# Kernel optimization log

Hardware: AMD Instinct MI355X
Metric: run time of the kernel (lower is better)

## Reference

```python
import jax, jax.numpy as jnp
import numpy as np

D_IN = 1024
D_OUT = 1024
NUM_HEADS = 16
HEAD_DIM = D_OUT // NUM_HEADS


def setup_inputs() -> dict:
    key = jax.random.key(0)
    ks = jax.random.split(key, 9)
    s = 0.02
    return {
        "x": jax.random.normal(ks[0], (2, 2048, D_IN), dtype=jnp.float32),
        "Wq": jax.random.normal(ks[1], (D_IN, D_OUT), dtype=jnp.float32) * s,
        "bq": jnp.zeros((D_OUT,), dtype=jnp.float32),
        "Wk": jax.random.normal(ks[2], (D_IN, D_OUT), dtype=jnp.float32) * s,
        "bk": jnp.zeros((D_OUT,), dtype=jnp.float32),
        "Wv": jax.random.normal(ks[3], (D_IN, D_OUT), dtype=jnp.float32) * s,
        "bv": jnp.zeros((D_OUT,), dtype=jnp.float32),
        "Wo": jax.random.normal(ks[4], (D_OUT, D_OUT), dtype=jnp.float32) * s,
        "bo": jnp.zeros((D_OUT,), dtype=jnp.float32),
    }


def reference(x, Wq, bq, Wk, bk, Wv, bv, Wo, bo):
    B, S, _ = x.shape
    H, Dh = NUM_HEADS, HEAD_DIM
    q = (x @ Wq + bq).reshape(B, S, H, Dh).transpose(0, 2, 1, 3)  # bhsd
    k = (x @ Wk + bk).reshape(B, S, H, Dh).transpose(0, 2, 1, 3)
    v = (x @ Wv + bv).reshape(B, S, H, Dh).transpose(0, 2, 1, 3)
    scores = jnp.einsum("bhqd,bhkd->bhqk", q, k) * (Dh ** -0.5)
    causal = jnp.tril(jnp.ones((S, S), dtype=bool))
    scores = jnp.where(causal, scores, jnp.float32(-jnp.inf))
    w = jax.nn.softmax(scores, axis=-1)
    ctx = jnp.einsum("bhqk,bhkd->bhqd", w, v)
    ctx = ctx.transpose(0, 2, 1, 3).reshape(B, S, H * Dh)
    return ctx @ Wo + bo
```

## Files before the change

kernel.cpp:

```cpp
#include <hip/hip_runtime.h>
#include <cmath>

#define D_IN 1024
#define D_OUT 1024
#define NUM_HEADS 16
#define HEAD_DIM 64
#define BATCH 2
#define SEQ 2048
#define GK 1024
#define KT 32
#define NT_K (GK / 64)

typedef __attribute__((ext_vector_type(8))) short short8;
typedef __attribute__((ext_vector_type(4))) short short4v;
typedef __attribute__((ext_vector_type(4))) float float4v;
typedef __attribute__((ext_vector_type(16))) float f32x16;
typedef __attribute__((ext_vector_type(2))) int int2v;

__device__ __forceinline__ unsigned short f2bf(float f) {
  unsigned int u = __builtin_bit_cast(unsigned int, f);
  unsigned int r = (u + 0x7FFFu + ((u >> 16) & 1u)) >> 16;
  return (unsigned short)r;
}
__device__ __forceinline__ float bf2f(unsigned short h) {
  return __builtin_bit_cast(float, (unsigned int)h << 16);
}

__device__ __forceinline__ unsigned int cvtpk(float lo, float hi) {
  unsigned int r;
  asm("v_cvt_pk_bf16_f32 %0, %1, %2" : "=v"(r) : "v"(lo), "v"(hi));
  return r;
}

__device__ __forceinline__ void async_copy16(void* lds, const void* g) {
  __builtin_amdgcn_global_load_lds(
      (const __attribute__((address_space(1))) unsigned int*)g,
      (__attribute__((address_space(3))) unsigned int*)lds, 16, 0, 0);
}

__global__ __launch_bounds__(256) void prep(
    const float* __restrict__ x, const float* __restrict__ Wq,
    const float* __restrict__ Wk, const float* __restrict__ Wv,
    const float* __restrict__ Wo, unsigned short* __restrict__ xb,
    unsigned short* __restrict__ wqkv_t, unsigned short* __restrict__ wo_t) {
  const int z = blockIdx.z;
  if (z == 4) {
    const int bid = blockIdx.y * 32 + blockIdx.x;
    const size_t i0 = ((size_t)bid * 256 + threadIdx.x) * 16;
#pragma unroll
    for (int half = 0; half < 2; ++half) {
      const size_t o = i0 + half * 8;
      float4 a = *(const float4*)(x + o);
      float4 b = *(const float4*)(x + o + 4);
      union { unsigned int d[4]; short8 v; } t;
      t.d[0] = cvtpk(a.x, a.y); t.d[1] = cvtpk(a.z, a.w);
      t.d[2] = cvtpk(b.x, b.y); t.d[3] = cvtpk(b.z, b.w);
      *(short8*)(xb + o) = t.v;
    }
    return;
  }
  const float* W = (z == 0) ? Wq : (z == 1) ? Wk : (z == 2) ? Wv : Wo;
  unsigned short* out = (z < 3) ? (wqkv_t + (size_t)z * 1024 * 1024) : wo_t;

  __shared__ float T[32][33];
  const int r = threadIdx.x >> 3;
  const int c4 = (threadIdx.x & 7) << 2;
  const int k0 = blockIdx.x * 32, n0 = blockIdx.y * 32;

  float4 v = *(const float4*)(W + (size_t)(k0 + r) * 1024 + n0 + c4);
  T[r][c4 + 0] = v.x; T[r][c4 + 1] = v.y; T[r][c4 + 2] = v.z; T[r][c4 + 3] = v.w;
  __syncthreads();

  union { unsigned short u[4]; short4v v4; } o;
#pragma unroll
  for (int i = 0; i < 4; ++i) o.u[i] = f2bf(T[c4 + i][r]);
  *(short4v*)(out + (size_t)(n0 + r) * 1024 + k0 + c4) = o.v4;
}

__device__ __forceinline__ void stage_tile(
    const unsigned short* __restrict__ A, const unsigned short* __restrict__ Bt,
    unsigned short* S, int buf, int bm, int bn, int k0, int wave, int lane) {
  unsigned short* As = S + buf * 16384;
  unsigned short* Bs = As + 8192;
#pragma unroll
  for (int t = 0; t < 4; ++t) {
    const int c = (wave * 4 + t) * 64 + lane;
    const int srow = c >> 3;
    const int sgc = ((c & 7) ^ (srow & 7)) * 8;
    async_copy16(As + (size_t)c * 8, A + (size_t)(bm + srow) * GK + k0 + sgc);
  }
#pragma unroll
  for (int t = 0; t < 4; ++t) {
    const int c = (wave * 4 + t) * 64 + lane;
    const int srow = c >> 3;
    const int sgc = ((c & 7) ^ (srow & 7)) * 8;
    async_copy16(Bs + (size_t)c * 8, Bt + (size_t)(bn + srow) * GK + k0 + sgc);
  }
}

__device__ __forceinline__ void gemm_core(
    const unsigned short* __restrict__ A, const unsigned short* __restrict__ Bt,
    unsigned short* S, int bm, int bn, float4v acc[4][4]) {
  const int tid = threadIdx.x;
  const int wave = tid >> 6, lane = tid & 63;
  const int quad = lane >> 4, l16 = lane & 15;
  const int wr = wave >> 1, wc = wave & 1;
  const int sw = l16 & 7;

  stage_tile(A, Bt, S, 0, bm, bn, 0, wave, lane);

  for (int t = 0; t < NT_K; ++t) {
    if (t + 1 < NT_K) {
      stage_tile(A, Bt, S, (t + 1) & 1, bm, bn, (t + 1) * 64, wave, lane);
      asm volatile("s_waitcnt vmcnt(8)" ::: "memory");
    } else {
      asm volatile("s_waitcnt vmcnt(0)" ::: "memory");
    }
    __builtin_amdgcn_sched_barrier(0);
    __builtin_amdgcn_s_barrier();
    __builtin_amdgcn_sched_barrier(0);

    const unsigned short* Asc = S + (t & 1) * 16384;
    const unsigned short* Bsc = Asc + 8192;
#pragma unroll
    for (int h = 0; h < 2; ++h) {
      short8 af[4], bfr[4];
#pragma unroll
      for (int i = 0; i < 4; ++i) {
        const int row = wr * 64 + i * 16 + l16;
        af[i] = *(const short8*)&Asc[((size_t)row * 8 + ((h * 4 + quad) ^ sw)) * 8];
      }
#pragma unroll
      for (int j = 0; j < 4; ++j) {
        const int row = wc * 64 + j * 16 + l16;
        bfr[j] = *(const short8*)&Bsc[((size_t)row * 8 + ((h * 4 + quad) ^ sw)) * 8];
      }
#pragma unroll
      for (int i = 0; i < 4; ++i)
#pragma unroll
        for (int j = 0; j < 4; ++j)
          acc[i][j] = __builtin_amdgcn_mfma_f32_16x16x32_bf16(af[i], bfr[j], acc[i][j], 0, 0, 0);
    }

    __builtin_amdgcn_sched_barrier(0);
    __builtin_amdgcn_s_barrier();
    __builtin_amdgcn_sched_barrier(0);
  }
}

__global__ __launch_bounds__(256) void gemm_qkv(
    const unsigned short* __restrict__ A, const unsigned short* __restrict__ Bt,
    const float* __restrict__ bq, const float* __restrict__ bk,
    const float* __restrict__ bv,
    unsigned short* __restrict__ qbuf, unsigned short* __restrict__ kblk,
    unsigned short* __restrict__ vblk) {
  __shared__ unsigned short SMEM[2 * 128 * 64 * 2];
  const int tid = threadIdx.x;
  const int wave = tid >> 6, lane = tid & 63;
  const int quad = lane >> 4, l16 = lane & 15;
  const int wr = wave >> 1, wc = wave & 1;

  const int lid = blockIdx.y * 32 + blockIdx.x;
  const int nid = (lid & 7) * 96 + (lid >> 3);
  const int bm = (nid & 31) * 128, bn = (nid >> 5) * 128;

  float4v acc[4][4] = {};
  gemm_core(A, Bt, SMEM, bm, bn, acc);

  __syncthreads();

  const int seg = bn >> 10;
  const int nb0 = bn & 1023;
  const float* bias = (seg == 0) ? bq : (seg == 1) ? bk : bv;
  const float scale = (seg == 0) ? 0.18033688011112043f : 1.0f;

#pragma unroll
  for (int j = 0; j < 4; ++j) {
    const int nl = wc * 64 + j * 16 + l16;
    const float bsv = bias[nb0 + nl];
#pragma unroll
    for (int i = 0; i < 4; ++i) {
#pragma unroll
      for (int r = 0; r < 4; ++r) {
        const int ml = wr * 64 + i * 16 + quad * 4 + r;
        SMEM[ml * 136 + nl] = f2bf((acc[i][j][r] + bsv) * scale);
      }
    }
  }
  __syncthreads();

  const int b = bm >> 11;
  const int s0 = bm & 2047;

  if (seg == 0) {
#pragma unroll
    for (int it = 0; it < 8; ++it) {
      const int linear = it * 256 + tid;
      const int d3 = linear & 7;
      const int sl = (linear >> 3) & 127;
      const int h = linear >> 10;
      const short8 vv = *(const short8*)&SMEM[sl * 136 + h * 64 + d3 * 8];
      const int bh = b * NUM_HEADS + (nb0 >> 6) + h;
      *(short8*)&qbuf[((size_t)bh * SEQ + s0 + sl) * HEAD_DIM + d3 * 8] = vv;
    }
  } else if (seg == 1) {
#pragma unroll
    for (int it = 0; it < 8; ++it) {
      const int linear = it * 256 + tid;
      const int key = linear & 31;
      const int hb = (linear >> 5) & 1;
      const int f = (linear >> 6) & 3;
      const int st = (linear >> 8) & 3;
      const int h = linear >> 10;
      const int ml = st * 32 + key;
      const int nl = h * 64 + f * 16 + hb * 8;
      const short8 vv = *(const short8*)&SMEM[ml * 136 + nl];
      const int bh = b * NUM_HEADS + (nb0 >> 6) + h;
      const int stg = (s0 >> 5) + st;
      *(short8*)&kblk[((size_t)bh * 64 + stg) * 2048 + f * 512 + hb * 256 + key * 8] = vv;
    }
  } else {
#pragma unroll
    for (int it = 0; it < 8; ++it) {
      const int linear = it * 256 + tid;
      const int d31 = linear & 31;
      const int s8 = (linear >> 5) & 1;
      const int dt = (linear >> 6) & 1;
      const int kk = (linear >> 7) & 1;
      const int st = (linear >> 8) & 3;
      const int h = linear >> 10;
      const int nl = h * 64 + dt * 32 + d31;
      const int mlb = st * 32 + kk * 16 + s8 * 8;
      union { unsigned short u[8]; short8 v; } vv;
#pragma unroll
      for (int s0i = 0; s0i < 8; ++s0i)
        vv.u[s0i] = SMEM[(mlb + s0i) * 136 + nl];
      const int bh = b * NUM_HEADS + (nb0 >> 6) + h;
      const int stg = (s0 >> 5) + st;
      *(short8*)&vblk[((size_t)bh * 64 + stg) * 2048 + (kk * 2 + dt) * 512 +
                      s8 * 256 + d31 * 8] = vv.v;
    }
  }
}

__global__ __launch_bounds__(256) void gemm_out(
    const unsigned short* __restrict__ A, const unsigned short* __restrict__ Bt,
    const float* __restrict__ bo, float* __restrict__ out) {
  __shared__ unsigned short S[2 * 128 * 64 * 2];
  const int wave = threadIdx.x >> 6, lane = threadIdx.x & 63;
  const int quad = lane >> 4, l16 = lane & 15;
  const int wr = wave >> 1, wc = wave & 1;

  const int lid = blockIdx.y * 32 + blockIdx.x;
  const int nid = (lid & 7) * 32 + (lid >> 3);
  const int bm = (nid & 31) * 128, bn = (nid >> 5) * 128;

  float4v acc[4][4] = {};
  gemm_core(A, Bt, S, bm, bn, acc);

#pragma unroll
  for (int j = 0; j < 4; ++j) {
    const int n = bn + wc * 64 + j * 16 + l16;
    const float bsv = bo[n];
#pragma unroll
    for (int i = 0; i < 4; ++i) {
#pragma unroll
      for (int r = 0; r < 4; ++r) {
        const int m = bm + wr * 64 + i * 16 + quad * 4 + r;
        out[(size_t)m * D_OUT + n] = acc[i][j][r] + bsv;
      }
    }
  }
}

#define OBS 72

__global__ __launch_bounds__(256) void attn_kernel(
    const unsigned short* __restrict__ qf, const unsigned short* __restrict__ kblk,
    const unsigned short* __restrict__ vblk, unsigned short* __restrict__ ctx) {
  __shared__ unsigned short OB[4 * 32 * OBS];
  __shared__ float LL[4 * 32];

  const int id = blockIdx.x;
  const int bh = id & 31;
  const int qblk = 63 - (id >> 5);
  const int qw0 = qblk * 32;
  const int tid = threadIdx.x;
  const int w = tid >> 6;
  const int lane = tid & 63;
  const int l32 = lane & 31;
  const int hi = lane >> 5;

  const int nt = qblk + 1;
  const int qch = (nt + 3) >> 2;
  const int t0 = w * qch;
  const int t1 = min(nt, t0 + qch);

  const size_t bh_base = (size_t)bh * SEQ * HEAD_DIM;
  const unsigned short* kb = kblk + bh_base + (size_t)lane * 8;
  const unsigned short* vb = vblk + bh_base + (size_t)lane * 8;

  short8 qfr[4];
  {
    const unsigned short* qrow =
        qf + bh_base + (size_t)(qw0 + l32) * HEAD_DIM + hi * 8;
#pragma unroll
    for (int f = 0; f < 4; ++f) qfr[f] = *(const short8*)(qrow + f * 16);
  }

  f32x16 O0 = {}, O1 = {};
  float l_part = 0.f;

  if (t0 < t1) {
    short8 kA[4], vA[4], kB[4], vB[4];

    auto load = [&](int kt, short8 kd[4], short8 vd[4]) {
      const size_t base = (size_t)kt * 2048;
#pragma unroll
      for (int f = 0; f < 4; ++f) kd[f] = *(const short8*)(kb + base + f * 512);
#pragma unroll
      for (int f = 0; f < 4; ++f) vd[f] = *(const short8*)(vb + base + f * 512);
    };

    auto step = [&](int kt, const short8 kd[4], const short8 vd[4], bool masked) {
      (void)kt;
      f32x16 s = {};
#pragma unroll
      for (int f = 0; f < 4; ++f)
        s = __builtin_amdgcn_mfma_f32_32x32x16_bf16(kd[f], qfr[f], s, 0, 0, 0);

      float p[16];
#pragma unroll
      for (int g = 0; g < 4; ++g)
#pragma unroll
        for (int r = 0; r < 4; ++r) {
          float sv = s[g * 4 + r];
          if (masked) {
            const int krow = r + 8 * g + 4 * hi;
            sv = (krow <= l32) ? sv : -1e30f;
          }
          const float pv = __builtin_exp2f(sv);
          p[g * 4 + r] = pv;
          l_part += pv;
        }

      unsigned int c[8];
#pragma unroll
      for (int g = 0; g < 4; ++g) {
        c[g * 2 + 0] = cvtpk(p[g * 4 + 0], p[g * 4 + 1]);
        c[g * 2 + 1] = cvtpk(p[g * 4 + 2], p[g * 4 + 3]);
      }
      {
        int2v r0 = __builtin_amdgcn_permlane32_swap((int)c[0], (int)c[2], false, false);
        c[0] = (unsigned int)r0.x; c[2] = (unsigned int)r0.y;
        int2v r1 = __builtin_amdgcn_permlane32_swap((int)c[1], (int)c[3], false, false);
        c[1] = (unsigned int)r1.x; c[3] = (unsigned int)r1.y;
        int2v r2 = __builtin_amdgcn_permlane32_swap((int)c[4], (int)c[6], false, false);
        c[4] = (unsigned int)r2.x; c[6] = (unsigned int)r2.y;
        int2v r3 = __builtin_amdgcn_permlane32_swap((int)c[5], (int)c[7], false, false);
        c[5] = (unsigned int)r3.x; c[7] = (unsigned int)r3.y;
      }
      union { unsigned int d[4]; short8 v; } pa0, pa1;
      pa0.d[0] = c[0]; pa0.d[1] = c[1]; pa0.d[2] = c[2]; pa0.d[3] = c[3];
      pa1.d[0] = c[4]; pa1.d[1] = c[5]; pa1.d[2] = c[6]; pa1.d[3] = c[7];

      O0 = __builtin_amdgcn_mfma_f32_32x32x16_bf16(pa0.v, vd[0], O0, 0, 0, 0);
      O1 = __builtin_amdgcn_mfma_f32_32x32x16_bf16(pa0.v, vd[1], O1, 0, 0, 0);
      O0 = __builtin_amdgcn_mfma_f32_32x32x16_bf16(pa1.v, vd[2], O0, 0, 0, 0);
      O1 = __builtin_amdgcn_mfma_f32_32x32x16_bf16(pa1.v, vd[3], O1, 0, 0, 0);
    };

    load(t0, kA, vA);
    int kt = t0;
    while (true) {
      const bool lastA = (kt == t1 - 1);
      if (!lastA) load(kt + 1, kB, vB);
      step(kt, kA, vA, kt == nt - 1);
      if (lastA) break;
      ++kt;
      const bool lastB = (kt == t1 - 1);
      if (!lastB) load(kt + 1, kA, vA);
      step(kt, kB, vB, kt == nt - 1);
      if (lastB) break;
      ++kt;
    }
  }

  const float lsum = l_part + __shfl_xor(l_part, 32);
  if (hi == 0) LL[w * 32 + l32] = lsum;
#pragma unroll
  for (int g = 0; g < 4; ++g)
#pragma unroll
    for (int r = 0; r < 4; ++r) {
      const int reg = g * 4 + r;
      const int row = r + 8 * g + 4 * hi;
      OB[(w * 32 + row) * OBS + l32] = f2bf(O0[reg]);
      OB[(w * 32 + row) * OBS + 32 + l32] = f2bf(O1[reg]);
    }

  __syncthreads();

  const int row = w * 8 + (lane >> 3);
  const int col0 = (lane & 7) * 8;
  float acc[8] = {};
#pragma unroll
  for (int u = 0; u < 4; ++u) {
    const short8 t = *(const short8*)&OB[(u * 32 + row) * OBS + col0];
#pragma unroll
    for (int i = 0; i < 8; ++i) acc[i] += bf2f((unsigned short)t[i]);
  }
  const float inv = 1.0f / (LL[row] + LL[32 + row] + LL[64 + row] + LL[96 + row]);
  union { unsigned short u[8]; short8 v; } o;
#pragma unroll
  for (int i = 0; i < 8; ++i) o.u[i] = f2bf(acc[i] * inv);
  const int b = bh >> 4, h = bh & 15;
  const int qg = qw0 + row;
  *(short8*)(ctx + ((size_t)b * SEQ + qg) * D_OUT + h * HEAD_DIM + col0) = o.v;
}

extern "C" void kernel_launch(void* const* d_in, const int* in_sizes, int n_in,
                              void* d_out, int out_size, void* d_ws, size_t ws_size,
                              hipStream_t stream) {
  const float* x  = (const float*)d_in[0];
  const float* Wq = (const float*)d_in[1];
  const float* bq = (const float*)d_in[2];
  const float* Wk = (const float*)d_in[3];
  const float* bk = (const float*)d_in[4];
  const float* Wv = (const float*)d_in[5];
  const float* bv = (const float*)d_in[6];
  const float* Wo = (const float*)d_in[7];
  const float* bo = (const float*)d_in[8];
  float* out = (float*)d_out;

  const int M = BATCH * SEQ;
  unsigned short* xb     = (unsigned short*)d_ws;
  unsigned short* wqkv_t = xb + (size_t)M * D_IN;
  unsigned short* wo_t   = wqkv_t + (size_t)3 * D_OUT * D_IN;
  unsigned short* qb     = wo_t + (size_t)D_OUT * D_OUT;
  unsigned short* kblk   = qb + (size_t)M * D_OUT;
  unsigned short* vblk   = kblk + (size_t)M * D_OUT;
  unsigned short* cb     = vblk + (size_t)M * D_OUT;

  prep<<<dim3(32, 32, 5), 256, 0, stream>>>(x, Wq, Wk, Wv, Wo, xb, wqkv_t, wo_t);
  gemm_qkv<<<dim3(M / 128, 3 * D_OUT / 128), 256, 0, stream>>>(
      xb, wqkv_t, bq, bk, bv, qb, kblk, vblk);
  attn_kernel<<<dim3(32 * 64), 256, 0, stream>>>(qb, kblk, vblk, cb);
  gemm_out<<<dim3(M / 128, D_OUT / 128), 256, 0, stream>>>(cb, wo_t, bo, out);
}
```

Before: 178.5 us.

## Process two 32-row query tiles per attention block to reuse K/V loads

Each attention workgroup now handles a 64-row query block, split into two 32-row sub-tiles, instead of a single 32-row tile. Every K/V tile loaded from global memory feeds both sub-tiles, which roughly halves K/V traffic per query row and halves the grid size. The cost is more accumulator registers, a larger LDS reduction buffer and fewer workgroups, which may lower occupancy and parallelism. The first sub-tile also sits idle on the final key tile.

```diff
diff --git a/kernel.cpp b/kernel.cpp
--- a/kernel.cpp
+++ b/kernel.cpp
@@ -278,20 +278,20 @@
 __global__ __launch_bounds__(256) void attn_kernel(
     const unsigned short* __restrict__ qf, const unsigned short* __restrict__ kblk,
     const unsigned short* __restrict__ vblk, unsigned short* __restrict__ ctx) {
-  __shared__ unsigned short OB[4 * 32 * OBS];
-  __shared__ float LL[4 * 32];
+  __shared__ unsigned short OB[4 * 64 * OBS];
+  __shared__ float LL[4 * 64];
 
   const int id = blockIdx.x;
   const int bh = id & 31;
-  const int qblk = 63 - (id >> 5);
-  const int qw0 = qblk * 32;
+  const int j = 31 - (id >> 5);
+  const int qw0 = j * 64;
   const int tid = threadIdx.x;
   const int w = tid >> 6;
   const int lane = tid & 63;
   const int l32 = lane & 31;
   const int hi = lane >> 5;
 
-  const int nt = qblk + 1;
+  const int nt = 2 * j + 2;
   const int qch = (nt + 3) >> 2;
   const int t0 = w * qch;
   const int t1 = min(nt, t0 + qch);
@@ -300,16 +300,17 @@
   const unsigned short* kb = kblk + bh_base + (size_t)lane * 8;
   const unsigned short* vb = vblk + bh_base + (size_t)lane * 8;
 
-  short8 qfr[4];
-  {
+  short8 qfr[2][4];
+#pragma unroll
+  for (int qt = 0; qt < 2; ++qt) {
     const unsigned short* qrow =
-        qf + bh_base + (size_t)(qw0 + l32) * HEAD_DIM + hi * 8;
-#pragma unroll
-    for (int f = 0; f < 4; ++f) qfr[f] = *(const short8*)(qrow + f * 16);
-  }
-
-  f32x16 O0 = {}, O1 = {};
-  float l_part = 0.f;
+        qf + bh_base + (size_t)(qw0 + qt * 32 + l32) * HEAD_DIM + hi * 8;
+#pragma unroll
+    for (int f = 0; f < 4; ++f) qfr[qt][f] = *(const short8*)(qrow + f * 16);
+  }
+
+  f32x16 O[2][2] = {};
+  float l_part[2] = {};
 
   if (t0 < t1) {
     short8 kA[4], vA[4], kB[4], vB[4];
@@ -322,52 +323,56 @@
       for (int f = 0; f < 4; ++f) vd[f] = *(const short8*)(vb + base + f * 512);
     };
 
-    auto step = [&](int kt, const short8 kd[4], const short8 vd[4], bool masked) {
-      (void)kt;
-      f32x16 s = {};
-#pragma unroll
-      for (int f = 0; f < 4; ++f)
-        s = __builtin_amdgcn_mfma_f32_32x32x16_bf16(kd[f], qfr[f], s, 0, 0, 0);
-
-      float p[16];
-#pragma unroll
-      for (int g = 0; g < 4; ++g)
-#pragma unroll
-        for (int r = 0; r < 4; ++r) {
-          float sv = s[g * 4 + r];
-          if (masked) {
-            const int krow = r + 8 * g + 4 * hi;
-            sv = (krow <= l32) ? sv : -1e30f;
+    auto step = [&](int kt, const short8 kd[4], const short8 vd[4]) {
+#pragma unroll
+      for (int qt = 0; qt < 2; ++qt) {
+        if (qt == 0 && kt > 2 * j) continue;
+        const bool masked = (kt == 2 * j + qt);
+        f32x16 s = {};
+#pragma unroll
+        for (int f = 0; f < 4; ++f)
+          s = __builtin_amdgcn_mfma_f32_32x32x16_bf16(kd[f], qfr[qt][f], s, 0, 0, 0);
+
+        float p[16];
+#pragma unroll
+        for (int g = 0; g < 4; ++g)
+#pragma unroll
+          for (int r = 0; r < 4; ++r) {
+            float sv = s[g * 4 + r];
+            if (masked) {
+              const int krow = r + 8 * g + 4 * hi;
+              sv = (krow <= l32) ? sv : -1e30f;
+            }
+            const float pv = __builtin_exp2f(sv);
+            p[g * 4 + r] = pv;
+            l_part[qt] += pv;
           }
-          const float pv = __builtin_exp2f(sv);
-          p[g * 4 + r] = pv;
-          l_part += pv;
+
+        unsigned int c[8];
+#pragma unroll
+        for (int g = 0; g < 4; ++g) {
+          c[g * 2 + 0] = cvtpk(p[g * 4 + 0], p[g * 4 + 1]);
+          c[g * 2 + 1] = cvtpk(p[g * 4 + 2], p[g * 4 + 3]);
         }
-
-      unsigned int c[8];
-#pragma unroll
-      for (int g = 0; g < 4; ++g) {
-        c[g * 2 + 0] = cvtpk(p[g * 4 + 0], p[g * 4 + 1]);
-        c[g * 2 + 1] = cvtpk(p[g * 4 + 2], p[g * 4 + 3]);
-      }
-      {
-        int2v r0 = __builtin_amdgcn_permlane32_swap((int)c[0], (int)c[2], false, false);
-        c[0] = (unsigned int)r0.x; c[2] = (unsigned int)r0.y;
-        int2v r1 = __builtin_amdgcn_permlane32_swap((int)c[1], (int)c[3], false, false);
-        c[1] = (unsigned int)r1.x; c[3] = (unsigned int)r1.y;
-        int2v r2 = __builtin_amdgcn_permlane32_swap((int)c[4], (int)c[6], false, false);
-        c[4] = (unsigned int)r2.x; c[6] = (unsigned int)r2.y;
-        int2v r3 = __builtin_amdgcn_permlane32_swap((int)c[5], (int)c[7], false, false);
-        c[5] = (unsigned int)r3.x; c[7] = (unsigned int)r3.y;
-      }
-      union { unsigned int d[4]; short8 v; } pa0, pa1;
-      pa0.d[0] = c[0]; pa0.d[1] = c[1]; pa0.d[2] = c[2]; pa0.d[3] = c[3];
-      pa1.d[0] = c[4]; pa1.d[1] = c[5]; pa1.d[2] = c[6]; pa1.d[3] = c[7];
-
-      O0 = __builtin_amdgcn_mfma_f32_32x32x16_bf16(pa0.v, vd[0], O0, 0, 0, 0);
-      O1 = __builtin_amdgcn_mfma_f32_32x32x16_bf16(pa0.v, vd[1], O1, 0, 0, 0);
-      O0 = __builtin_amdgcn_mfma_f32_32x32x16_bf16(pa1.v, vd[2], O0, 0, 0, 0);
-      O1 = __builtin_amdgcn_mfma_f32_32x32x16_bf16(pa1.v, vd[3], O1, 0, 0, 0);
+        {
+          int2v r0 = __builtin_amdgcn_permlane32_swap((int)c[0], (int)c[2], false, false);
+          c[0] = (unsigned int)r0.x; c[2] = (unsigned int)r0.y;
+          int2v r1 = __builtin_amdgcn_permlane32_swap((int)c[1], (int)c[3], false, false);
+          c[1] = (unsigned int)r1.x; c[3] = (unsigned int)r1.y;
+          int2v r2 = __builtin_amdgcn_permlane32_swap((int)c[4], (int)c[6], false, false);
+          c[4] = (unsigned int)r2.x; c[6] = (unsigned int)r2.y;
+          int2v r3 = __builtin_amdgcn_permlane32_swap((int)c[5], (int)c[7], false, false);
+          c[5] = (unsigned int)r3.x; c[7] = (unsigned int)r3.y;
+        }
+        union { unsigned int d[4]; short8 v; } pa0, pa1;
+        pa0.d[0] = c[0]; pa0.d[1] = c[1]; pa0.d[2] = c[2]; pa0.d[3] = c[3];
+        pa1.d[0] = c[4]; pa1.d[1] = c[5]; pa1.d[2] = c[6]; pa1.d[3] = c[7];
+
+        O[qt][0] = __builtin_amdgcn_mfma_f32_32x32x16_bf16(pa0.v, vd[0], O[qt][0], 0, 0, 0);
+        O[qt][1] = __builtin_amdgcn_mfma_f32_32x32x16_bf16(pa0.v, vd[1], O[qt][1], 0, 0, 0);
+        O[qt][0] = __builtin_amdgcn_mfma_f32_32x32x16_bf16(pa1.v, vd[2], O[qt][0], 0, 0, 0);
+        O[qt][1] = __builtin_amdgcn_mfma_f32_32x32x16_bf16(pa1.v, vd[3], O[qt][1], 0, 0, 0);
+      }
     };
 
     load(t0, kA, vA);
@@ -375,47 +380,55 @@
     while (true) {
       const bool lastA = (kt == t1 - 1);
       if (!lastA) load(kt + 1, kB, vB);
-      step(kt, kA, vA, kt == nt - 1);
+      step(kt, kA, vA);
       if (lastA) break;
       ++kt;
       const bool lastB = (kt == t1 - 1);
       if (!lastB) load(kt + 1, kA, vA);
-      step(kt, kB, vB, kt == nt - 1);
+      step(kt, kB, vB);
       if (lastB) break;
       ++kt;
     }
   }
 
-  const float lsum = l_part + __shfl_xor(l_part, 32);
-  if (hi == 0) LL[w * 32 + l32] = lsum;
-#pragma unroll
-  for (int g = 0; g < 4; ++g)
-#pragma unroll
-    for (int r = 0; r < 4; ++r) {
-      const int reg = g * 4 + r;
-      const int row = r + 8 * g + 4 * hi;
-      OB[(w * 32 + row) * OBS + l32] = f2bf(O0[reg]);
-      OB[(w * 32 + row) * OBS + 32 + l32] = f2bf(O1[reg]);
-    }
+#pragma unroll
+  for (int qt = 0; qt < 2; ++qt) {
+    const float lsum = l_part[qt] + __shfl_xor(l_part[qt], 32);
+    if (hi == 0) LL[w * 64 + qt * 32 + l32] = lsum;
+#pragma unroll
+    for (int g = 0; g < 4; ++g)
+#pragma unroll
+      for (int r = 0; r < 4; ++r) {
+        const int reg = g * 4 + r;
+        const int row = qt * 32 + r + 8 * g + 4 * hi;
+        OB[(w * 64 + row) * OBS + l32] = f2bf(O[qt][0][reg]);
+        OB[(w * 64 + row) * OBS + 32 + l32] = f2bf(O[qt][1][reg]);
+      }
+  }
 
   __syncthreads();
 
-  const int row = w * 8 + (lane >> 3);
-  const int col0 = (lane & 7) * 8;
-  float acc[8] = {};
-#pragma unroll
-  for (int u = 0; u < 4; ++u) {
-    const short8 t = *(const short8*)&OB[(u * 32 + row) * OBS + col0];
-#pragma unroll
-    for (int i = 0; i < 8; ++i) acc[i] += bf2f((unsigned short)t[i]);
-  }
-  const float inv = 1.0f / (LL[row] + LL[32 + row] + LL[64 + row] + LL[96 + row]);
-  union { unsigned short u[8]; short8 v; } o;
-#pragma unroll
-  for (int i = 0; i < 8; ++i) o.u[i] = f2bf(acc[i] * inv);
   const int b = bh >> 4, h = bh & 15;
-  const int qg = qw0 + row;
-  *(short8*)(ctx + ((size_t)b * SEQ + qg) * D_OUT + h * HEAD_DIM + col0) = o.v;
+#pragma unroll
+  for (int rep = 0; rep < 2; ++rep) {
+    const int idx = rep * 256 + tid;
+    const int row = idx >> 3;
+    const int col0 = (idx & 7) * 8;
+    float acc[8] = {};
+#pragma unroll
+    for (int u = 0; u < 4; ++u) {
+      const short8 t = *(const short8*)&OB[(u * 64 + row) * OBS + col0];
+#pragma unroll
+      for (int i = 0; i < 8; ++i) acc[i] += bf2f((unsigned short)t[i]);
+    }
+    const float inv =
+        1.0f / (LL[row] + LL[64 + row] + LL[128 + row] + LL[192 + row]);
+    union { unsigned short u[8]; short8 v; } o;
+#pragma unroll
+    for (int i = 0; i < 8; ++i) o.u[i] = f2bf(acc[i] * inv);
+    const int qg = qw0 + row;
+    *(short8*)(ctx + ((size_t)b * SEQ + qg) * D_OUT + h * HEAD_DIM + col0) = o.v;
+  }
 }
 
 extern "C" void kernel_launch(void* const* d_in, const int* in_sizes, int n_in,
@@ -444,6 +457,6 @@
   prep<<<dim3(32, 32, 5), 256, 0, stream>>>(x, Wq, Wk, Wv, Wo, xb, wqkv_t, wo_t);
   gemm_qkv<<<dim3(M / 128, 3 * D_OUT / 128), 256, 0, stream>>>(
       xb, wqkv_t, bq, bk, bv, qb, kblk, vblk);
-  attn_kernel<<<dim3(32 * 64), 256, 0, stream>>>(qb, kblk, vblk, cb);
+  attn_kernel<<<dim3(32 * 32), 256, 0, stream>>>(qb, kblk, vblk, cb);
   gemm_out<<<dim3(M / 128, D_OUT / 128), 256, 0, stream>>>(cb, wo_t, bo, out);
 }
```

Result: no change. 178.3 us (-0.1%).
